# Kernel optimization log

Measured on AMD Instinct MI355X. Metric: run time of the kernel, lower is better.

Reference implementation:

```python
import jax, jax.numpy as jnp
import numpy as np

DIM = 1024
HEAD_DIM = 64
N_HEADS = DIM // HEAD_DIM  # 16
COND_DIM = 256
LENGTHS = (1, 4, 16, 64, 256, 1024)
SEQ = sum(LENGTHS)  # 1365
LN_EPS = 1e-5
ROT_D = 3 * (HEAD_DIM // 8)  # 24; 2*ROT_D = 48 <= HEAD_DIM


def _axial_pos(h, w):
    hp = np.linspace(-1.0, 1.0, h + 1); hp = (hp[:-1] + hp[1:]) / 2
    wp = np.linspace(-1.0, 1.0, w + 1); wp = (wp[:-1] + wp[1:]) / 2
    return np.stack(np.meshgrid(hp, wp, indexing='ij'), -1).reshape(h * w, 2)


def _make_theta():
    d = 5
    poses = []
    for i in range(d):
        pa = _axial_pos(32 >> i, 32 >> i)
        pr = np.full((pa.shape[0], 1), (d - i) / d)
        poses.insert(0, np.concatenate([pa, pr], -1))
    poses.insert(0, np.zeros((1, 3)))
    pos = np.concatenate(poses, 0)  # [1365, 3]
    log_min, log_max = np.log(np.pi), np.log(10 * np.pi)
    freqs = np.exp(np.linspace(log_min, log_max, HEAD_DIM // 8 * N_HEADS + 1)[:-1])
    freqs = freqs.reshape(HEAD_DIM // 8, N_HEADS).T  # [H, head_dim//8]
    th = pos[:, None, 0:1] * freqs  # [S, H, head_dim//8]
    tw = pos[:, None, 1:2] * freqs
    td = pos[:, None, 2:3] * freqs
    theta = np.concatenate([th, tw, td], -1)  # [S, H, ROT_D]
    return jnp.asarray(theta.transpose(1, 0, 2), dtype=jnp.float32)  # [H, S, ROT_D]


def _make_mask():
    m = np.zeros((SEQ, SEQ), dtype=bool)
    i = 0
    for L in LENGTHS:
        m[i:, i:i + L] = True
        i += L
    return jnp.asarray(m)


THETA = _make_theta()  # [H, S, ROT_D], constant buffer
MASK = _make_mask()    # [S, S] bool, constant buffer


def _rope(x, theta):
    # x: [B, H, S, head_dim]; theta: [H, S, ROT_D]
    d = theta.shape[-1]
    x1, x2, rest = x[..., :d], x[..., d:2 * d], x[..., 2 * d:]
    cos, sin = jnp.cos(theta), jnp.sin(theta)
    return jnp.concatenate([x1 * cos - x2 * sin, x2 * cos + x1 * sin, rest], -1)


def setup_inputs() -> dict:
    key = jax.random.key(0)
    ks = jax.random.split(key, 6)
    s = 0.02
    x = jax.random.normal(ks[0], (8, SEQ, DIM), jnp.float32)
    cond = jax.random.normal(ks[1], (8, 1, COND_DIM), jnp.float32)
    adaln_w = jax.random.normal(ks[2], (COND_DIM, 2 * DIM), jnp.float32) * s
    adaln_b = jnp.zeros((2 * DIM,), jnp.float32)
    qkv_w = jax.random.normal(ks[3], (DIM, 3 * DIM), jnp.float32) * s
    qkv_b = jnp.zeros((3 * DIM,), jnp.float32)
    out_w = jax.random.normal(ks[4], (DIM, DIM), jnp.float32) * s
    out_b = jnp.zeros((DIM,), jnp.float32)
    return {"x": x, "cond": cond, "adaln_w": adaln_w, "adaln_b": adaln_b,
            "qkv_w": qkv_w, "qkv_b": qkv_b, "out_w": out_w, "out_b": out_b}


def reference(x, cond, adaln_w, adaln_b, qkv_w, qkv_b, out_w, out_b):
    B, S, _ = x.shape
    skip = x
    # AdaLN: zero-init proj in the original; math is LN(x)*(w+1)+b
    wb = cond @ adaln_w + adaln_b  # [B, 1, 2*DIM]
    w, b = jnp.split(wb, 2, axis=-1)
    mu = x.mean(-1, keepdims=True)
    var = ((x - mu) ** 2).mean(-1, keepdims=True)
    xn = (x - mu) * jax.lax.rsqrt(var + LN_EPS)
    xn = xn * (w + 1.0) + b
    # QKV
    qkv = xn @ qkv_w + qkv_b  # [B, S, 3*DIM]
    qkv = qkv.reshape(B, S, 3, N_HEADS, HEAD_DIM).transpose(0, 3, 2, 1, 4)  # [B,H,3,S,hd]
    q, k, v = qkv[:, :, 0], qkv[:, :, 1], qkv[:, :, 2]
    theta = THETA[:, :S]  # [H, S, ROT_D]
    q = _rope(q, theta)
    k = _rope(k, theta)
    # block-causal masked SDPA
    scores = jnp.einsum('bhqd,bhkd->bhqk', q, k) / np.sqrt(HEAD_DIM).astype(np.float32)
    scores = jnp.where(MASK[:S, :S], scores, -1e30)
    attn = jax.nn.softmax(scores, axis=-1)
    o = jnp.einsum('bhqk,bhkd->bhqd', attn, v)
    o = o.transpose(0, 2, 1, 3).reshape(B, S, DIM)
    return o @ out_w + out_b + skip
```

## Files before the change

kernel.cpp:

```cpp
#include <hip/hip_runtime.h>
#include <math.h>


typedef unsigned short u16;
typedef unsigned short u16x8 __attribute__((ext_vector_type(8)));
typedef unsigned short u16x4 __attribute__((ext_vector_type(4)));
typedef __bf16        bf16x8 __attribute__((ext_vector_type(8)));
typedef float         f32x4  __attribute__((ext_vector_type(4)));

#define SEQ  1365
#define SP   1408
#define BHN  128
#define MTOT 10920
#define DIMN 1024
#define QSCALE 0.1803368801111204f

__device__ __forceinline__ u16 f2bf(float x){
  unsigned r; asm("v_cvt_pk_bf16_f32 %0, %1, %1" : "=v"(r) : "v"(x));
  return (u16)r;
}
__device__ __forceinline__ unsigned cvtpk(float a, float b){
  unsigned r; asm("v_cvt_pk_bf16_f32 %0, %1, %2" : "=v"(r) : "v"(a), "v"(b));
  return r;
}
__device__ __forceinline__ float bf2f(u16 b){
  return __builtin_bit_cast(float, ((unsigned)b) << 16);
}
__device__ __forceinline__ bf16x8 ldbf8(const u16* p){
  return __builtin_bit_cast(bf16x8, *(const u16x8*)p);
}
__device__ __forceinline__ f32x4 mfma16(bf16x8 a, bf16x8 b, f32x4 c){
  return __builtin_amdgcn_mfma_f32_16x16x32_bf16(a, b, c, 0, 0, 0);
}
__device__ __forceinline__ void gload16(const u16* g, u16* l){
  __builtin_amdgcn_global_load_lds(
      (const __attribute__((address_space(1))) void*)(g),
      (__attribute__((address_space(3))) void*)(l), 16, 0, 0);
}

__global__ __launch_bounds__(256) void transpose_bf16(const float* __restrict__ in,
                                                      u16* __restrict__ outT,
                                                      int K, int N){
  __shared__ float tile[32][33];
  const int tx = threadIdx.x & 31, ty = threadIdx.x >> 5;
  const int n0 = blockIdx.x*32, k0 = blockIdx.y*32;
#pragma unroll
  for (int i=0;i<32;i+=8) tile[ty+i][tx] = in[(size_t)(k0+ty+i)*N + n0+tx];
  __syncthreads();
#pragma unroll
  for (int i=0;i<32;i+=8) outT[(size_t)(n0+ty+i)*K + k0+tx] = f2bf(tile[tx][ty+i]);
}

__global__ __launch_bounds__(256) void adaln_kernel(const float* __restrict__ cond,
                                                    const float* __restrict__ w,
                                                    const float* __restrict__ bsrc,
                                                    float* __restrict__ wb){
  __shared__ float cs[256];
  const int bt = blockIdx.x >> 3, ch = blockIdx.x & 7;
  const int t = threadIdx.x;
  cs[t] = cond[bt*256 + t];
  __syncthreads();
  const int n = ch*256 + t;
  float acc = bsrc[n];
  for (int j=0;j<256;j++) acc += cs[j] * w[(size_t)j*2048 + n];
  wb[bt*2048 + n] = acc;
}

__global__ __launch_bounds__(256) void theta_kernel(float* __restrict__ ctab,
                                                    float* __restrict__ stab){
  int idx = blockIdx.x*256 + threadIdx.x;
  if (idx >= 16*SEQ*24) return;
  int c = idx % 24;
  int rest = idx / 24;
  int s = rest % SEQ;
  int h = rest / SEQ;
  float p0 = 0.f, p1 = 0.f, p2 = 0.f;
  if (s >= 1){
    int start, sh; float pr;
    if      (s <   5){start=1;   sh=1; pr=0.2f;}
    else if (s <  21){start=5;   sh=2; pr=0.4f;}
    else if (s <  85){start=21;  sh=3; pr=0.6f;}
    else if (s < 341){start=85;  sh=4; pr=0.8f;}
    else             {start=341; sh=5; pr=1.0f;}
    int n = s - start;
    int row = n >> sh, colp = n & ((1<<sh)-1);
    float g = (float)(1 << sh);
    p0 = -1.f + (2*row+1)/g;
    p1 = -1.f + (2*colp+1)/g;
    p2 = pr;
  }
  int j = c & 7, comp = c >> 3;
  float kf = (float)(j*16 + h);
  float freq = 3.14159265358979323846f * exp2f(kf * (3.3219280948873623f/128.f));
  float pos = (comp==0) ? p0 : ((comp==1) ? p1 : p2);
  float th = pos * freq;
  ctab[idx] = cosf(th);
  stab[idx] = sinf(th);
}

__global__ __launch_bounds__(256) void ln_kernel(const float* __restrict__ x,
                                                 const float* __restrict__ wb,
                                                 u16* __restrict__ xn){
  const int row = blockIdx.x;
  const int b = row / SEQ;
  const int t = threadIdx.x, w = t>>6, l = t&63;
  const float4 v = ((const float4*)(x + (size_t)row*DIMN))[t];
  float s = v.x + v.y + v.z + v.w;
#pragma unroll
  for (int m=1; m<64; m<<=1) s += __shfl_xor(s, m);
  __shared__ float red1[4], red2[4];
  if (l == 0) red1[w] = s;
  __syncthreads();
  float mean = (red1[0]+red1[1]+red1[2]+red1[3]) * (1.f/1024.f);
  float dx = v.x-mean, dy = v.y-mean, dz = v.z-mean, dw = v.w-mean;
  float q = dx*dx + dy*dy + dz*dz + dw*dw;
#pragma unroll
  for (int m=1; m<64; m<<=1) q += __shfl_xor(q, m);
  if (l == 0) red2[w] = q;
  __syncthreads();
  float var = (red2[0]+red2[1]+red2[2]+red2[3]) * (1.f/1024.f);
  float rs = rsqrtf(var + 1e-5f);
  const float* wrow = wb + b*2048;
  int n0 = t*4;
  u16x4 o;
  o[0] = f2bf(dx*rs*(wrow[n0+0]+1.f) + wrow[1024+n0+0]);
  o[1] = f2bf(dy*rs*(wrow[n0+1]+1.f) + wrow[1024+n0+1]);
  o[2] = f2bf(dz*rs*(wrow[n0+2]+1.f) + wrow[1024+n0+2]);
  o[3] = f2bf(dw*rs*(wrow[n0+3]+1.f) + wrow[1024+n0+3]);
  *(u16x4*)&xn[(size_t)row*DIMN + n0] = o;
}

__global__ __launch_bounds__(256) void gemm_qkv(const u16* __restrict__ A,
                                                const u16* __restrict__ BT,
                                                const float* __restrict__ bias,
                                                u16* __restrict__ qb, u16* __restrict__ kb,
                                                u16* __restrict__ vb){
  __shared__ u16 As[128*32];
  __shared__ u16 Bs[128*32];
  const int K = 1024;
  const int t = threadIdx.x, l = t & 63, w = t >> 6, lr = l & 15, lg = l >> 4;
  const int wr = (w>>1)*64, wc = (w&1)*64;
  const int bm = blockIdx.y*128, bn = blockIdx.x*128;

  f32x4 acc[4][4];
#pragma unroll
  for (int mi=0;mi<4;mi++)
#pragma unroll
    for (int ni=0;ni<4;ni++) acc[mi][ni] = (f32x4){0.f,0.f,0.f,0.f};

  const int srow = l >> 2;
  const int scol = (l & 3) << 3;

  for (int k0=0; k0<K; k0+=32){
    __syncthreads();
#pragma unroll
    for (int j=0;j<2;j++){
      int rb = (w*2+j)*16;
      int gr = bm + rb + srow; if (gr >= MTOT) gr = MTOT-1;
      gload16(&A[(size_t)gr*K + k0 + scol], &As[rb*32]);
      gload16(&BT[(size_t)(bn + rb + srow)*K + k0 + scol], &Bs[rb*32]);
    }
    __syncthreads();
    bf16x8 af[4], bfr[4];
#pragma unroll
    for (int mi=0;mi<4;mi++) af[mi] = ldbf8(&As[(wr+mi*16+lr)*32 + lg*8]);
#pragma unroll
    for (int ni=0;ni<4;ni++) bfr[ni] = ldbf8(&Bs[(wc+ni*16+lr)*32 + lg*8]);
#pragma unroll
    for (int mi=0;mi<4;mi++)
#pragma unroll
      for (int ni=0;ni<4;ni++)
        acc[mi][ni] = mfma16(af[mi], bfr[ni], acc[mi][ni]);
  }

#pragma unroll
  for (int mi=0;mi<4;mi++)
#pragma unroll
    for (int ni=0;ni<4;ni++){
      int col = bn + wc + ni*16 + lr;
      float bia = bias[col];
      int three = col >> 10, rem = col & 1023;
      int h = rem >> 6, d = rem & 63;
      float scl = (three == 0) ? QSCALE : 1.0f;
#pragma unroll
      for (int r=0;r<4;r++){
        int m = bm + wr + mi*16 + lg*4 + r;
        if (m < MTOT){
          int b = m / SEQ; int s = m - b*SEQ;
          u16 val = f2bf((acc[mi][ni][r] + bia) * scl);
          int bh = b*16 + h;
          if (three == 0)      qb[((size_t)bh*SP + s)*64 + d] = val;
          else if (three == 1) kb[((size_t)bh*SP + s)*64 + d] = val;
          else                 vb[((size_t)bh*64 + d)*SP + s] = val;
        }
      }
    }
}

__global__ __launch_bounds__(256) void rope2_kernel(u16* __restrict__ qb,
                                                    u16* __restrict__ kb,
                                                    const float* __restrict__ ctab,
                                                    const float* __restrict__ stab){
  int rid = blockIdx.x*256 + threadIdx.x;
  if (rid >= BHN*SEQ) return;
  int bh = rid / SEQ, s = rid - bh*SEQ, h = bh & 15;
  const float* cp = ctab + (size_t)(h*SEQ + s)*24;
  const float* sp = stab + (size_t)(h*SEQ + s)*24;
  float cs[24], sn[24];
#pragma unroll
  for (int i=0;i<6;i++){
    ((float4*)cs)[i] = ((const float4*)cp)[i];
    ((float4*)sn)[i] = ((const float4*)sp)[i];
  }
  size_t base = ((size_t)bh*SP + s)*64;
  u16 buf[48];
#pragma unroll
  for (int i=0;i<6;i++) ((u16x8*)buf)[i] = *(const u16x8*)&qb[base + i*8];
#pragma unroll
  for (int j=0;j<24;j++){
    float x1 = bf2f(buf[j]), x2 = bf2f(buf[24+j]);
    buf[j]    = f2bf(x1*cs[j] - x2*sn[j]);
    buf[24+j] = f2bf(x2*cs[j] + x1*sn[j]);
  }
#pragma unroll
  for (int i=0;i<6;i++) *(u16x8*)&qb[base + i*8] = ((u16x8*)buf)[i];
#pragma unroll
  for (int i=0;i<6;i++) ((u16x8*)buf)[i] = *(const u16x8*)&kb[base + i*8];
#pragma unroll
  for (int j=0;j<24;j++){
    float x1 = bf2f(buf[j]), x2 = bf2f(buf[24+j]);
    buf[j]    = f2bf(x1*cs[j] - x2*sn[j]);
    buf[24+j] = f2bf(x2*cs[j] + x1*sn[j]);
  }
#pragma unroll
  for (int i=0;i<6;i++) *(u16x8*)&kb[base + i*8] = ((u16x8*)buf)[i];
}

__global__ __launch_bounds__(256) void attn_kernel(const u16* __restrict__ qb,
                                                   const u16* __restrict__ kb,
                                                   const u16* __restrict__ vb,
                                                   u16* __restrict__ ob){
  __shared__ u16 Ks[64*72];
  __shared__ u16 Vs[64*72];
  __shared__ u16 Ps[128*72];
  const int bx = blockIdx.x;
  const int qt = (bx < 9) ? (bx + 2) : (bx - 9);
  const int bh = blockIdx.y;
  const int t = threadIdx.x, w = t>>6, l = t&63, lr = l&15, lg = l>>4, lg4 = lg<<2;
  const u16* qB = qb + (size_t)bh*SP*64;
  const u16* kB = kb + (size_t)bh*SP*64;
  const u16* vB = vb + (size_t)bh*64*SP;
  const int q0 = qt*128 + w*32;

  bf16x8 qf[2][2];
#pragma unroll
  for (int ni=0; ni<2; ni++)
#pragma unroll
    for (int kk=0; kk<2; kk++)
      qf[ni][kk] = ldbf8(&qB[(size_t)(q0+ni*16+lr)*64 + kk*32 + lg*8]);
  const int qg0 = q0 + lr, qg1 = q0 + 16 + lr;

  f32x4 oacc[2][4];
#pragma unroll
  for (int mo=0;mo<2;mo++)
#pragma unroll
    for (int nd=0;nd<4;nd++) oacc[mo][nd] = (f32x4){0.f,0.f,0.f,0.f};
  float lst[2] = {0.f, 0.f};

  int qmax = min(qt*128+127, SEQ-1);
  int kend = (qmax<1)?1:(qmax<5)?5:(qmax<21)?21:(qmax<85)?85:(qmax<341)?341:SEQ;
  int nkt = (kend + 63) >> 6;

  for (int kt=0; kt<nkt; kt++){
    const int kbase = kt*64;
    __syncthreads();
#pragma unroll
    for (int j=0;j<2;j++){
      int flat = t + j*256;
      int row = flat >> 3, kc = (flat & 7) << 3;
      *(u16x8*)&Ks[row*72+kc] = *(const u16x8*)&kB[(size_t)(kbase+row)*64 + kc];
      *(u16x8*)&Vs[row*72+kc] = *(const u16x8*)&vB[(size_t)row*SP + kbase + kc];
    }
    __syncthreads();

    f32x4 sacc[4][2];
#pragma unroll
    for (int mi=0;mi<4;mi++){
      sacc[mi][0] = (f32x4){0.f,0.f,0.f,0.f};
      sacc[mi][1] = (f32x4){0.f,0.f,0.f,0.f};
    }
#pragma unroll
    for (int mi=0;mi<4;mi++){
      bf16x8 k0f = ldbf8(&Ks[(mi*16+lr)*72 + lg*8]);
      bf16x8 k1f = ldbf8(&Ks[(mi*16+lr)*72 + 32 + lg*8]);
      sacc[mi][0] = mfma16(k0f, qf[0][0], sacc[mi][0]);
      sacc[mi][0] = mfma16(k1f, qf[0][1], sacc[mi][0]);
      sacc[mi][1] = mfma16(k0f, qf[1][0], sacc[mi][1]);
      sacc[mi][1] = mfma16(k1f, qf[1][1], sacc[mi][1]);
    }

    int lastk = kbase + 63;
    int visLast = (lastk>=SEQ)?(1<<30):(lastk>=341)?341:(lastk>=85)?85:
                  (lastk>=21)?21:(lastk>=5)?5:(lastk>=1)?1:0;
    if (visLast > q0){
#pragma unroll
      for (int mi=0;mi<4;mi++){
        int kv = kbase + mi*16 + lg4;
#pragma unroll
        for (int r=0;r<4;r++){
          int key = kv + r;
          int visv = (key>=SEQ)?(1<<30):(key>=341)?341:(key>=85)?85:
                     (key>=21)?21:(key>=5)?5:(key>=1)?1:0;
          if (qg0 < visv) sacc[mi][0][r] = -1e30f;
          if (qg1 < visv) sacc[mi][1][r] = -1e30f;
        }
      }
    }

    float pa[2] = {0.f, 0.f}, pb[2] = {0.f, 0.f};
#pragma unroll
    for (int mi=0;mi<4;mi++)
#pragma unroll
      for (int ni=0;ni<2;ni++){
        float p0 = __builtin_amdgcn_exp2f(sacc[mi][ni][0]);
        float p1 = __builtin_amdgcn_exp2f(sacc[mi][ni][1]);
        float p2 = __builtin_amdgcn_exp2f(sacc[mi][ni][2]);
        float p3 = __builtin_amdgcn_exp2f(sacc[mi][ni][3]);
        pa[ni] += p0 + p1;
        pb[ni] += p2 + p3;
        uint2 pk = { cvtpk(p0, p1), cvtpk(p2, p3) };
        *(uint2*)&Ps[(w*32+ni*16+lr)*72 + mi*16 + lg4] = pk;
      }
#pragma unroll
    for (int ni=0;ni<2;ni++){
      float s = pa[ni] + pb[ni];
      s += __shfl_xor(s, 16);
      s += __shfl_xor(s, 32);
      lst[ni] += s;
    }

    bf16x8 pf[2][2];
#pragma unroll
    for (int mo=0;mo<2;mo++)
#pragma unroll
      for (int kk=0;kk<2;kk++)
        pf[mo][kk] = ldbf8(&Ps[(w*32+mo*16+lr)*72 + kk*32 + lg*8]);
#pragma unroll
    for (int nd=0;nd<4;nd++){
      bf16x8 v0 = ldbf8(&Vs[(nd*16+lr)*72 + lg*8]);
      bf16x8 v1 = ldbf8(&Vs[(nd*16+lr)*72 + 32 + lg*8]);
#pragma unroll
      for (int mo=0;mo<2;mo++){
        oacc[mo][nd] = mfma16(pf[mo][0], v0, oacc[mo][nd]);
        oacc[mo][nd] = mfma16(pf[mo][1], v1, oacc[mo][nd]);
      }
    }
  }

  const int b = bh >> 4, h = bh & 15;
  float linv[2][4];
#pragma unroll
  for (int mo=0;mo<2;mo++)
#pragma unroll
    for (int r=0;r<4;r++)
      linv[mo][r] = 1.f / __shfl(lst[mo], lg4 + r);
#pragma unroll
  for (int mo=0;mo<2;mo++)
#pragma unroll
    for (int r=0;r<4;r++){
      int p = q0 + mo*16 + lg4 + r;
      if (p < SEQ){
#pragma unroll
        for (int nd=0;nd<4;nd++)
          ob[((size_t)(b*SEQ + p))*DIMN + h*64 + nd*16 + lr] = f2bf(oacc[mo][nd][r] * linv[mo][r]);
      }
    }
}

__global__ __launch_bounds__(256) void gemm_out(const u16* __restrict__ A,
                                                const u16* __restrict__ BT,
                                                const float* __restrict__ bias,
                                                const float* __restrict__ skip,
                                                float* __restrict__ out){
  __shared__ u16 As[128*32];
  __shared__ u16 Bs[128*32];
  const int K = 1024;
  const int t = threadIdx.x, l = t & 63, w = t >> 6, lr = l & 15, lg = l >> 4;
  const int wr = (w>>1)*64, wc = (w&1)*64;
  const int bm = blockIdx.y*128, bn = blockIdx.x*128;

  f32x4 acc[4][4];
#pragma unroll
  for (int mi=0;mi<4;mi++)
#pragma unroll
    for (int ni=0;ni<4;ni++) acc[mi][ni] = (f32x4){0.f,0.f,0.f,0.f};

  const int srow = l >> 2;
  const int scol = (l & 3) << 3;

  for (int k0=0; k0<K; k0+=32){
    __syncthreads();
#pragma unroll
    for (int j=0;j<2;j++){
      int rb = (w*2+j)*16;
      int gr = bm + rb + srow; if (gr >= MTOT) gr = MTOT-1;
      gload16(&A[(size_t)gr*K + k0 + scol], &As[rb*32]);
      gload16(&BT[(size_t)(bn + rb + srow)*K + k0 + scol], &Bs[rb*32]);
    }
    __syncthreads();
    bf16x8 af[4], bfr[4];
#pragma unroll
    for (int mi=0;mi<4;mi++) af[mi] = ldbf8(&As[(wr+mi*16+lr)*32 + lg*8]);
#pragma unroll
    for (int ni=0;ni<4;ni++) bfr[ni] = ldbf8(&Bs[(wc+ni*16+lr)*32 + lg*8]);
#pragma unroll
    for (int mi=0;mi<4;mi++)
#pragma unroll
      for (int ni=0;ni<4;ni++)
        acc[mi][ni] = mfma16(af[mi], bfr[ni], acc[mi][ni]);
  }

#pragma unroll
  for (int mi=0;mi<4;mi++)
#pragma unroll
    for (int ni=0;ni<4;ni++){
      int col = bn + wc + ni*16 + lr;
      float bia = bias[col];
#pragma unroll
      for (int r=0;r<4;r++){
        int m = bm + wr + mi*16 + lg*4 + r;
        if (m < MTOT){
          size_t idx = (size_t)m*DIMN + col;
          out[idx] = acc[mi][ni][r] + bia + skip[idx];
        }
      }
    }
}

extern "C" void kernel_launch(void* const* d_in, const int* in_sizes, int n_in,
                              void* d_out, int out_size, void* d_ws, size_t ws_size,
                              hipStream_t stream) {
  (void)in_sizes; (void)n_in; (void)out_size; (void)ws_size;
  const float* x        = (const float*)d_in[0];
  const float* cond     = (const float*)d_in[1];
  const float* adaln_w  = (const float*)d_in[2];
  const float* adaln_b  = (const float*)d_in[3];
  const float* qkv_w    = (const float*)d_in[4];
  const float* qkv_b    = (const float*)d_in[5];
  const float* out_w    = (const float*)d_in[6];
  const float* out_b    = (const float*)d_in[7];
  float* out = (float*)d_out;

  char* ws = (char*)d_ws;
  size_t off = 0;
  auto alloc = [&](size_t bytes)->void*{
    void* p = ws + off;
    off += (bytes + 255) & ~(size_t)255;
    return p;
  };
  float* wb     = (float*)alloc((size_t)8*2048*4);
  u16*   xn     = (u16*)  alloc((size_t)MTOT*DIMN*2);
  u16*   qkv_wT = (u16*)  alloc((size_t)3072*1024*2);
  u16*   out_wT = (u16*)  alloc((size_t)1024*1024*2);
  u16*   qbuf   = (u16*)  alloc((size_t)BHN*SP*64*2);
  u16*   kbuf   = (u16*)  alloc((size_t)BHN*SP*64*2);
  u16*   vbuf   = (u16*)  alloc((size_t)BHN*SP*64*2);
  float* ctab   = (float*)alloc((size_t)16*SEQ*24*4);
  float* stab   = (float*)alloc((size_t)16*SEQ*24*4);
  u16*   obuf   = xn;

  transpose_bf16<<<dim3(3072/32, 1024/32), 256, 0, stream>>>(qkv_w, qkv_wT, 1024, 3072);
  transpose_bf16<<<dim3(1024/32, 1024/32), 256, 0, stream>>>(out_w, out_wT, 1024, 1024);
  theta_kernel<<<(16*SEQ*24 + 255)/256, 256, 0, stream>>>(ctab, stab);
  adaln_kernel<<<64, 256, 0, stream>>>(cond, adaln_w, adaln_b, wb);
  ln_kernel<<<MTOT, 256, 0, stream>>>(x, wb, xn);
  gemm_qkv<<<dim3(3072/128, (MTOT+127)/128), 256, 0, stream>>>(xn, qkv_wT, qkv_b, qbuf, kbuf, vbuf);
  rope2_kernel<<<(BHN*SEQ + 255)/256, 256, 0, stream>>>(qbuf, kbuf, ctab, stab);
  attn_kernel<<<dim3((SEQ+127)/128, BHN), 256, 0, stream>>>(qbuf, kbuf, vbuf, obuf);
  gemm_out<<<dim3(1024/128, (MTOT+127)/128), 256, 0, stream>>>(obuf, out_wT, out_b, x, out);
}
```

Before: 440.0 us.

## Rewrite QKV and output GEMMs with 192x256 tiles, double-buffered LDS, XCD-aware mapping

Both GEMMs move from 128x128 tiles with a K-step of 32 and single-buffered LDS to 192x256 tiles, 512 threads, and a K-step of 64 with double-buffered async global-to-LDS loads. LDS uses an XOR swizzle to avoid bank conflicts, and s_setprio and explicit waitcnt are used to overlap loads with MFMA work. A 1-D grid is remapped so neighbouring tiles land on the same XCD for L2 reuse. The goal is to cut global and LDS traffic per FLOP and hide load latency. The cost is larger register and LDS use, plus some padding waste on the M edge.

```diff
diff --git a/kernel.cpp b/kernel.cpp
--- a/kernel.cpp
+++ b/kernel.cpp
@@ -29,6 +29,9 @@
 __device__ __forceinline__ bf16x8 ldbf8(const u16* p){
   return __builtin_bit_cast(bf16x8, *(const u16x8*)p);
 }
+__device__ __forceinline__ bf16x8 ldsv(const char* p){
+  return __builtin_bit_cast(bf16x8, *(const u16x8*)p);
+}
 __device__ __forceinline__ f32x4 mfma16(bf16x8 a, bf16x8 b, f32x4 c){
   return __builtin_amdgcn_mfma_f32_16x16x32_bf16(a, b, c, 0, 0, 0);
 }
@@ -36,6 +39,19 @@
   __builtin_amdgcn_global_load_lds(
       (const __attribute__((address_space(1))) void*)(g),
       (__attribute__((address_space(3))) void*)(l), 16, 0, 0);
+}
+
+__device__ __forceinline__ void stage7(const u16* sA0, const u16* sA1, const u16* sA2,
+                                       const u16* sB0, const u16* sB1,
+                                       const u16* sB2, const u16* sB3,
+                                       int koff, u16* dA, u16* dB, int w){
+  gload16(sA0 + koff, dA +          w*512);
+  gload16(sA1 + koff, dA +  4096 +  w*512);
+  gload16(sA2 + koff, dA +  8192 +  w*512);
+  gload16(sB0 + koff, dB +          w*512);
+  gload16(sB1 + koff, dB +  4096 +  w*512);
+  gload16(sB2 + koff, dB +  8192 +  w*512);
+  gload16(sB3 + koff, dB + 12288 +  w*512);
 }
 
 __global__ __launch_bounds__(256) void transpose_bf16(const float* __restrict__ in,
@@ -130,61 +146,107 @@
   *(u16x4*)&xn[(size_t)row*DIMN + n0] = o;
 }
 
-__global__ __launch_bounds__(256) void gemm_qkv(const u16* __restrict__ A,
-                                                const u16* __restrict__ BT,
-                                                const float* __restrict__ bias,
-                                                u16* __restrict__ qb, u16* __restrict__ kb,
-                                                u16* __restrict__ vb){
-  __shared__ u16 As[128*32];
-  __shared__ u16 Bs[128*32];
-  const int K = 1024;
-  const int t = threadIdx.x, l = t & 63, w = t >> 6, lr = l & 15, lg = l >> 4;
-  const int wr = (w>>1)*64, wc = (w&1)*64;
-  const int bm = blockIdx.y*128, bn = blockIdx.x*128;
-
-  f32x4 acc[4][4];
-#pragma unroll
-  for (int mi=0;mi<4;mi++)
+
+__global__ __launch_bounds__(512, 2) void gemm_qkv(const u16* __restrict__ A,
+                                                   const u16* __restrict__ BT,
+                                                   const float* __restrict__ bias,
+                                                   u16* __restrict__ qb, u16* __restrict__ kb,
+                                                   u16* __restrict__ vb){
+  __shared__ u16 As[2][12288];
+  __shared__ u16 Bs[2][16384];
+  const int t = threadIdx.x, l = t & 63, w = t >> 6;
+  const int lr = l & 15, lg = l >> 4;
+  const int wr = w >> 2, wc = w & 3;
+
+  const int orig = blockIdx.x;
+  const int xcd = orig & 7, idx = orig >> 3;
+  const int wg = (xcd < 4) ? xcd*86 + idx : 344 + (xcd-4)*85 + idx;
+  const int mt = wg / 12, nt = wg - mt*12;
+  const int bm = mt*192, bn = nt*256;
+
+  const int row8 = l >> 3;
+  const int gch  = (l & 7) ^ row8;
+  int grA0 = bm +   0 + w*8 + row8; if (grA0 >= MTOT) grA0 = MTOT-1;
+  int grA1 = bm +  64 + w*8 + row8; if (grA1 >= MTOT) grA1 = MTOT-1;
+  int grA2 = bm + 128 + w*8 + row8; if (grA2 >= MTOT) grA2 = MTOT-1;
+  const u16* sA0 = A + (size_t)grA0*1024 + gch*8;
+  const u16* sA1 = A + (size_t)grA1*1024 + gch*8;
+  const u16* sA2 = A + (size_t)grA2*1024 + gch*8;
+  const u16* sB0 = BT + (size_t)(bn +   0 + w*8 + row8)*1024 + gch*8;
+  const u16* sB1 = BT + (size_t)(bn +  64 + w*8 + row8)*1024 + gch*8;
+  const u16* sB2 = BT + (size_t)(bn + 128 + w*8 + row8)*1024 + gch*8;
+  const u16* sB3 = BT + (size_t)(bn + 192 + w*8 + row8)*1024 + gch*8;
+
+  const int pch  = (lg ^ (lr & 7)) << 4;
+  const int aoff = (wr*96 + lr)*128 + pch;
+  const int boff = (wc*64 + lr)*128 + pch;
+
+  f32x4 acc[6][4];
+#pragma unroll
+  for (int mi=0;mi<6;mi++)
 #pragma unroll
     for (int ni=0;ni<4;ni++) acc[mi][ni] = (f32x4){0.f,0.f,0.f,0.f};
 
-  const int srow = l >> 2;
-  const int scol = (l & 3) << 3;
-
-  for (int k0=0; k0<K; k0+=32){
-    __syncthreads();
-#pragma unroll
-    for (int j=0;j<2;j++){
-      int rb = (w*2+j)*16;
-      int gr = bm + rb + srow; if (gr >= MTOT) gr = MTOT-1;
-      gload16(&A[(size_t)gr*K + k0 + scol], &As[rb*32]);
-      gload16(&BT[(size_t)(bn + rb + srow)*K + k0 + scol], &Bs[rb*32]);
-    }
-    __syncthreads();
-    bf16x8 af[4], bfr[4];
-#pragma unroll
-    for (int mi=0;mi<4;mi++) af[mi] = ldbf8(&As[(wr+mi*16+lr)*32 + lg*8]);
-#pragma unroll
-    for (int ni=0;ni<4;ni++) bfr[ni] = ldbf8(&Bs[(wc+ni*16+lr)*32 + lg*8]);
-#pragma unroll
-    for (int mi=0;mi<4;mi++)
+  stage7(sA0,sA1,sA2,sB0,sB1,sB2,sB3, 0,   As[0], Bs[0], w);
+  stage7(sA0,sA1,sA2,sB0,sB1,sB2,sB3, 64,  As[1], Bs[1], w);
+  asm volatile("s_waitcnt vmcnt(7)" ::: "memory");
+  __builtin_amdgcn_s_barrier();
+  __builtin_amdgcn_sched_barrier(0);
+
+#pragma unroll 2
+  for (int kt = 0; kt < 16; ++kt){
+    const int bi = kt & 1;
+    const char* Ab = (const char*)As[bi];
+    const char* Bb = (const char*)Bs[bi];
+    bf16x8 a0[6], b0[4], a1[6], b1[4];
+#pragma unroll
+    for (int mi=0;mi<6;mi++) a0[mi] = ldsv(Ab + (aoff + mi*2048));
+#pragma unroll
+    for (int ni=0;ni<4;ni++) b0[ni] = ldsv(Bb + (boff + ni*2048));
+#pragma unroll
+    for (int mi=0;mi<6;mi++) a1[mi] = ldsv(Ab + ((aoff + mi*2048) ^ 64));
+#pragma unroll
+    for (int ni=0;ni<4;ni++) b1[ni] = ldsv(Bb + ((boff + ni*2048) ^ 64));
+    __builtin_amdgcn_s_setprio(1);
+#pragma unroll
+    for (int mi=0;mi<6;mi++)
 #pragma unroll
       for (int ni=0;ni<4;ni++)
-        acc[mi][ni] = mfma16(af[mi], bfr[ni], acc[mi][ni]);
-  }
-
-#pragma unroll
-  for (int mi=0;mi<4;mi++)
+        acc[mi][ni] = mfma16(a0[mi], b0[ni], acc[mi][ni]);
+    __builtin_amdgcn_s_setprio(0);
+    asm volatile("s_waitcnt lgkmcnt(0)" ::: "memory");
+    __builtin_amdgcn_s_barrier();
+    __builtin_amdgcn_sched_barrier(0);
+    if (kt < 14)
+      stage7(sA0,sA1,sA2,sB0,sB1,sB2,sB3, (kt+2)*64, As[bi], Bs[bi], w);
+    __builtin_amdgcn_sched_barrier(0);
+    __builtin_amdgcn_s_setprio(1);
+#pragma unroll
+    for (int mi=0;mi<6;mi++)
+#pragma unroll
+      for (int ni=0;ni<4;ni++)
+        acc[mi][ni] = mfma16(a1[mi], b1[ni], acc[mi][ni]);
+    __builtin_amdgcn_s_setprio(0);
+    if (kt < 15){
+      if (kt < 14) asm volatile("s_waitcnt vmcnt(7)" ::: "memory");
+      else         asm volatile("s_waitcnt vmcnt(0)" ::: "memory");
+      __builtin_amdgcn_s_barrier();
+      __builtin_amdgcn_sched_barrier(0);
+    }
+  }
+
+#pragma unroll
+  for (int mi=0;mi<6;mi++)
 #pragma unroll
     for (int ni=0;ni<4;ni++){
-      int col = bn + wc + ni*16 + lr;
+      int col = bn + wc*64 + ni*16 + lr;
       float bia = bias[col];
       int three = col >> 10, rem = col & 1023;
       int h = rem >> 6, d = rem & 63;
       float scl = (three == 0) ? QSCALE : 1.0f;
 #pragma unroll
       for (int r=0;r<4;r++){
-        int m = bm + wr + mi*16 + lg*4 + r;
+        int m = bm + wr*96 + mi*16 + lg*4 + r;
         if (m < MTOT){
           int b = m / SEQ; int s = m - b*SEQ;
           u16 val = f2bf((acc[mi][ni][r] + bia) * scl);
@@ -377,61 +439,106 @@
     }
 }
 
-__global__ __launch_bounds__(256) void gemm_out(const u16* __restrict__ A,
-                                                const u16* __restrict__ BT,
-                                                const float* __restrict__ bias,
-                                                const float* __restrict__ skip,
-                                                float* __restrict__ out){
-  __shared__ u16 As[128*32];
-  __shared__ u16 Bs[128*32];
-  const int K = 1024;
-  const int t = threadIdx.x, l = t & 63, w = t >> 6, lr = l & 15, lg = l >> 4;
-  const int wr = (w>>1)*64, wc = (w&1)*64;
-  const int bm = blockIdx.y*128, bn = blockIdx.x*128;
-
-  f32x4 acc[4][4];
-#pragma unroll
-  for (int mi=0;mi<4;mi++)
+__global__ __launch_bounds__(512, 2) void gemm_out(const u16* __restrict__ A,
+                                                   const u16* __restrict__ BT,
+                                                   const float* __restrict__ bias,
+                                                   const float* __restrict__ skip,
+                                                   float* __restrict__ out){
+  __shared__ u16 As[2][12288];
+  __shared__ u16 Bs[2][16384];
+  const int t = threadIdx.x, l = t & 63, w = t >> 6;
+  const int lr = l & 15, lg = l >> 4;
+  const int wr = w >> 2, wc = w & 3;
+
+  const int orig = blockIdx.x;
+  const int xcd = orig & 7, idx = orig >> 3;
+  const int wg = (xcd < 4) ? xcd*29 + idx : 116 + (xcd-4)*28 + idx;
+  const int mt = wg >> 2, nt = wg & 3;
+  const int bm = mt*192, bn = nt*256;
+
+  const int row8 = l >> 3;
+  const int gch  = (l & 7) ^ row8;
+  int grA0 = bm +   0 + w*8 + row8; if (grA0 >= MTOT) grA0 = MTOT-1;
+  int grA1 = bm +  64 + w*8 + row8; if (grA1 >= MTOT) grA1 = MTOT-1;
+  int grA2 = bm + 128 + w*8 + row8; if (grA2 >= MTOT) grA2 = MTOT-1;
+  const u16* sA0 = A + (size_t)grA0*1024 + gch*8;
+  const u16* sA1 = A + (size_t)grA1*1024 + gch*8;
+  const u16* sA2 = A + (size_t)grA2*1024 + gch*8;
+  const u16* sB0 = BT + (size_t)(bn +   0 + w*8 + row8)*1024 + gch*8;
+  const u16* sB1 = BT + (size_t)(bn +  64 + w*8 + row8)*1024 + gch*8;
+  const u16* sB2 = BT + (size_t)(bn + 128 + w*8 + row8)*1024 + gch*8;
+  const u16* sB3 = BT + (size_t)(bn + 192 + w*8 + row8)*1024 + gch*8;
+
+  const int pch  = (lg ^ (lr & 7)) << 4;
+  const int aoff = (wr*96 + lr)*128 + pch;
+  const int boff = (wc*64 + lr)*128 + pch;
+
+  f32x4 acc[6][4];
+#pragma unroll
+  for (int mi=0;mi<6;mi++)
 #pragma unroll
     for (int ni=0;ni<4;ni++) acc[mi][ni] = (f32x4){0.f,0.f,0.f,0.f};
 
-  const int srow = l >> 2;
-  const int scol = (l & 3) << 3;
-
-  for (int k0=0; k0<K; k0+=32){
-    __syncthreads();
-#pragma unroll
-    for (int j=0;j<2;j++){
-      int rb = (w*2+j)*16;
-      int gr = bm + rb + srow; if (gr >= MTOT) gr = MTOT-1;
-      gload16(&A[(size_t)gr*K + k0 + scol], &As[rb*32]);
-      gload16(&BT[(size_t)(bn + rb + srow)*K + k0 + scol], &Bs[rb*32]);
-    }
-    __syncthreads();
-    bf16x8 af[4], bfr[4];
-#pragma unroll
-    for (int mi=0;mi<4;mi++) af[mi] = ldbf8(&As[(wr+mi*16+lr)*32 + lg*8]);
-#pragma unroll
-    for (int ni=0;ni<4;ni++) bfr[ni] = ldbf8(&Bs[(wc+ni*16+lr)*32 + lg*8]);
-#pragma unroll
-    for (int mi=0;mi<4;mi++)
+  stage7(sA0,sA1,sA2,sB0,sB1,sB2,sB3, 0,   As[0], Bs[0], w);
+  stage7(sA0,sA1,sA2,sB0,sB1,sB2,sB3, 64,  As[1], Bs[1], w);
+  asm volatile("s_waitcnt vmcnt(7)" ::: "memory");
+  __builtin_amdgcn_s_barrier();
+  __builtin_amdgcn_sched_barrier(0);
+
+#pragma unroll 2
+  for (int kt = 0; kt < 16; ++kt){
+    const int bi = kt & 1;
+    const char* Ab = (const char*)As[bi];
+    const char* Bb = (const char*)Bs[bi];
+    bf16x8 a0[6], b0[4], a1[6], b1[4];
+#pragma unroll
+    for (int mi=0;mi<6;mi++) a0[mi] = ldsv(Ab + (aoff + mi*2048));
+#pragma unroll
+    for (int ni=0;ni<4;ni++) b0[ni] = ldsv(Bb + (boff + ni*2048));
+#pragma unroll
+    for (int mi=0;mi<6;mi++) a1[mi] = ldsv(Ab + ((aoff + mi*2048) ^ 64));
+#pragma unroll
+    for (int ni=0;ni<4;ni++) b1[ni] = ldsv(Bb + ((boff + ni*2048) ^ 64));
+    __builtin_amdgcn_s_setprio(1);
+#pragma unroll
+    for (int mi=0;mi<6;mi++)
 #pragma unroll
       for (int ni=0;ni<4;ni++)
-        acc[mi][ni] = mfma16(af[mi], bfr[ni], acc[mi][ni]);
-  }
-
-#pragma unroll
-  for (int mi=0;mi<4;mi++)
+        acc[mi][ni] = mfma16(a0[mi], b0[ni], acc[mi][ni]);
+    __builtin_amdgcn_s_setprio(0);
+    asm volatile("s_waitcnt lgkmcnt(0)" ::: "memory");
+    __builtin_amdgcn_s_barrier();
+    __builtin_amdgcn_sched_barrier(0);
+    if (kt < 14)
+      stage7(sA0,sA1,sA2,sB0,sB1,sB2,sB3, (kt+2)*64, As[bi], Bs[bi], w);
+    __builtin_amdgcn_sched_barrier(0);
+    __builtin_amdgcn_s_setprio(1);
+#pragma unroll
+    for (int mi=0;mi<6;mi++)
+#pragma unroll
+      for (int ni=0;ni<4;ni++)
+        acc[mi][ni] = mfma16(a1[mi], b1[ni], acc[mi][ni]);
+    __builtin_amdgcn_s_setprio(0);
+    if (kt < 15){
+      if (kt < 14) asm volatile("s_waitcnt vmcnt(7)" ::: "memory");
+      else         asm volatile("s_waitcnt vmcnt(0)" ::: "memory");
+      __builtin_amdgcn_s_barrier();
+      __builtin_amdgcn_sched_barrier(0);
+    }
+  }
+
+#pragma unroll
+  for (int mi=0;mi<6;mi++)
 #pragma unroll
     for (int ni=0;ni<4;ni++){
-      int col = bn + wc + ni*16 + lr;
+      int col = bn + wc*64 + ni*16 + lr;
       float bia = bias[col];
 #pragma unroll
       for (int r=0;r<4;r++){
-        int m = bm + wr + mi*16 + lg*4 + r;
+        int m = bm + wr*96 + mi*16 + lg*4 + r;
         if (m < MTOT){
-          size_t idx = (size_t)m*DIMN + col;
-          out[idx] = acc[mi][ni][r] + bia + skip[idx];
+          size_t idx2 = (size_t)m*DIMN + col;
+          out[idx2] = acc[mi][ni][r] + bia + skip[idx2];
         }
       }
     }
@@ -474,8 +581,8 @@
   theta_kernel<<<(16*SEQ*24 + 255)/256, 256, 0, stream>>>(ctab, stab);
   adaln_kernel<<<64, 256, 0, stream>>>(cond, adaln_w, adaln_b, wb);
   ln_kernel<<<MTOT, 256, 0, stream>>>(x, wb, xn);
-  gemm_qkv<<<dim3(3072/128, (MTOT+127)/128), 256, 0, stream>>>(xn, qkv_wT, qkv_b, qbuf, kbuf, vbuf);
+  gemm_qkv<<<684, 512, 0, stream>>>(xn, qkv_wT, qkv_b, qbuf, kbuf, vbuf);
   rope2_kernel<<<(BHN*SEQ + 255)/256, 256, 0, stream>>>(qbuf, kbuf, ctab, stab);
   attn_kernel<<<dim3((SEQ+127)/128, BHN), 256, 0, stream>>>(qbuf, kbuf, vbuf, obuf);
-  gemm_out<<<dim3(1024/128, (MTOT+127)/128), 256, 0, stream>>>(obuf, out_wT, out_b, x, out);
-}
+  gemm_out<<<228, 512, 0, stream>>>(obuf, out_wT, out_b, x, out);
+}
```

Result: no change. 445.6 us (+1.3%).
